# Optimization experiments

Measured on AMD Instinct MI355X. Metric: run time of the kernel, lower is better.

Reference implementation:

```python
import jax, jax.numpy as jnp
import numpy as np
import math

B, T, HIDDEN = 1, 2048, 2048
N_HEADS, N_KV = 16, 8
HD = HIDDEN // N_HEADS  # 128
EPS = 1e-6
THETA = 1e6


def _rmsnorm(x, w, eps=EPS):
    return x * jax.lax.rsqrt(jnp.mean(x * x, axis=-1, keepdims=True) + eps) * w


def _rope(x, sin, cos):
    # even/odd split, non-interleaved concat output (matches get_rope)
    x1 = x[..., 0::2]
    x2 = x[..., 1::2]
    s = sin[None, :, None, :]  # [1, T, 1, HD//2]
    c = cos[None, :, None, :]
    return jnp.concatenate([x1 * c - x2 * s, x1 * s + x2 * c], axis=-1)


def setup_inputs() -> dict:
    key = jax.random.key(0)
    ks = jax.random.split(key, 6)
    x = jax.random.normal(ks[0], (B, T, HIDDEN), dtype=jnp.float32)
    Wq = 0.02 * jax.random.normal(ks[1], (HIDDEN, 2 * HIDDEN), dtype=jnp.float32)
    Wk = 0.02 * jax.random.normal(ks[2], (HIDDEN, N_KV * HD), dtype=jnp.float32)
    Wv = 0.02 * jax.random.normal(ks[3], (HIDDEN, N_KV * HD), dtype=jnp.float32)
    Wo = 0.02 * jax.random.normal(ks[4], (2 * HIDDEN, HIDDEN), dtype=jnp.float32)
    q_norm_w = jnp.ones((2 * HD,), dtype=jnp.float32)
    k_norm_w = jnp.ones((HD,), dtype=jnp.float32)
    inv_freq = 1.0 / (THETA ** (jnp.arange(0, HD, 2, dtype=jnp.float32) / HD))
    freqs = jnp.arange(T, dtype=jnp.float32)[:, None] * inv_freq[None, :]  # [T, HD//2]
    return {"x": x, "Wq": Wq, "Wk": Wk, "Wv": Wv, "Wo": Wo,
            "q_norm_w": q_norm_w, "k_norm_w": k_norm_w,
            "sin": jnp.sin(freqs), "cos": jnp.cos(freqs)}


def reference(x, Wq, Wk, Wv, Wo, q_norm_w, k_norm_w, sin, cos):
    b, t, _ = x.shape
    # projections
    q = (x @ Wq).reshape(b, t, N_HEADS, 2 * HD)
    k = (x @ Wk).reshape(b, t, N_KV, HD)
    v = (x @ Wv).reshape(b, t, N_KV, HD)
    # per-head QK RMSNorm (q_norm over 2*head_dim)
    q = _rmsnorm(q, q_norm_w)
    k = _rmsnorm(k, k_norm_w)
    # split q into 2*N_HEADS attention heads of dim HD, apply RoPE
    hq = 2 * N_HEADS
    q = _rope(q.reshape(b, t, hq, HD), sin, cos)
    k = _rope(k, sin, cos)
    # GQA: repeat kv heads
    g = hq // N_KV
    k = jnp.repeat(k, g, axis=2)  # [b, t, hq, HD]
    v = jnp.repeat(v, g, axis=2)
    # attention: no causal mask in the original module
    att = jnp.einsum('bqhd,bkhd->bhqk', q, k) / math.sqrt(HD)
    p = jax.nn.softmax(att, axis=-1)
    out = jnp.einsum('bhqk,bkhd->bqhd', p, v).reshape(b, t, hq * HD)
    return out @ Wo
```

## Files before the change

kernel.cpp:

```cpp
#include <hip/hip_runtime.h>

typedef unsigned short u16;
typedef __attribute__((ext_vector_type(8))) short bf16x8;
typedef __attribute__((ext_vector_type(4))) short s16x4;
typedef __attribute__((ext_vector_type(4))) float f32x4;

__device__ __forceinline__ float bf2f(u16 u) {
  union { unsigned u; float f; } c; c.u = ((unsigned)u) << 16; return c.f;
}
__device__ __forceinline__ u16 f2bf(float f) {
  union { float f; unsigned u; } c; c.f = f;
  return (u16)((c.u + 0x7fffu + ((c.u >> 16) & 1u)) >> 16);
}
#if __has_builtin(__builtin_amdgcn_cvt_pk_bf16_f32)
__device__ __forceinline__ unsigned pkbf(float a, float b) {
  auto v = __builtin_amdgcn_cvt_pk_bf16_f32(a, b);
  return __builtin_bit_cast(unsigned, v);
}
#else
__device__ __forceinline__ unsigned pkbf(float a, float b) {
  return (unsigned)f2bf(a) | ((unsigned)f2bf(b) << 16);
}
#endif
#if __has_builtin(__builtin_amdgcn_mfma_f32_16x16x16bf16_1k)
#define MFMA16(a, b, c) __builtin_amdgcn_mfma_f32_16x16x16bf16_1k(a, b, c, 0, 0, 0)
#define HAVE_MFMA16 1
#endif
#if __has_builtin(__builtin_amdgcn_exp2f)
#define EXP2(x) __builtin_amdgcn_exp2f(x)
#else
#define EXP2(x) __expf((x) * 0.69314718f)
#endif
__device__ __forceinline__ void gl2lds16(const u16* g, u16* l) {
  __builtin_amdgcn_global_load_lds(
      (const __attribute__((address_space(1))) void*)g,
      (__attribute__((address_space(3))) void*)l, 16, 0, 0);
}

__device__ __forceinline__ void tr_cast_tile(const float* __restrict__ in,
                                             u16* __restrict__ out,
                                             int ldin, int ldout, int bx, int by) {
  __shared__ u16 tile[64][66];
  const int tx = threadIdx.x;
  const int lr = tx & 31, lc = tx >> 5;
  const int r0 = by << 6, c0 = bx << 6;
#pragma unroll
  for (int i = 0; i < 8; ++i) {
    int r = lc + (i << 3);
    float2 v = *(const float2*)&in[(size_t)(r0 + r) * ldin + c0 + (lr << 1)];
    *(unsigned*)&tile[r][lr << 1] = pkbf(v.x, v.y);
  }
  __syncthreads();
#pragma unroll
  for (int i = 0; i < 8; ++i) {
    int c = lc + (i << 3);
    unsigned v = (unsigned)tile[lr << 1][c] | ((unsigned)tile[(lr << 1) + 1][c] << 16);
    *(unsigned*)&out[(size_t)(c0 + c) * ldout + r0 + (lr << 1)] = v;
  }
}

__global__ __launch_bounds__(256) void prep(const float* __restrict__ x,
                                            u16* __restrict__ xb,
                                            const float* __restrict__ Wq,
                                            u16* __restrict__ WqT,
                                            const float* __restrict__ Wk,
                                            u16* __restrict__ WkT,
                                            const float* __restrict__ Wv,
                                            u16* __restrict__ WvT) {
  int b = blockIdx.x;
  if (b < 2048) {
    int i = (b * 256 + threadIdx.x) * 8;
    float4 a = *(const float4*)&x[i];
    float4 c = *(const float4*)&x[i + 4];
    union { unsigned u[4]; bf16x8 v; } w;
    w.u[0] = pkbf(a.x, a.y); w.u[1] = pkbf(a.z, a.w);
    w.u[2] = pkbf(c.x, c.y); w.u[3] = pkbf(c.z, c.w);
    *(bf16x8*)&xb[i] = w.v;
  } else if (b < 4096) {
    int t = b - 2048;
    tr_cast_tile(Wq, WqT, 4096, 2048, t & 63, t >> 6);
  } else if (b < 4608) {
    int t = b - 4096;
    tr_cast_tile(Wk, WkT, 1024, 2048, t & 15, t >> 4);
  } else {
    int t = b - 4608;
    tr_cast_tile(Wv, WvT, 1024, 2048, t & 15, t >> 4);
  }
}

__global__ __launch_bounds__(256) void transpose_cast(const float* __restrict__ in,
                                                      u16* __restrict__ out,
                                                      int ldin, int ldout) {
  tr_cast_tile(in, out, ldin, ldout, blockIdx.x, blockIdx.y);
}

__global__ __launch_bounds__(256) void gemm_bt(const u16* __restrict__ A,
                                               const u16* __restrict__ BT,
                                               u16* __restrict__ C,
                                               int M, int N, int K) {
  __shared__ u16 Asl[2][128 * 32];
  __shared__ u16 Bsl[2][128 * 32];
  const int tid = threadIdx.x;
  const int lane = tid & 63, wv = tid >> 6;
  const int lr = lane & 15, qd = lane >> 4;
  const int wr = wv >> 1, wc = wv & 1;
  const int m0 = blockIdx.y << 7, n0 = blockIdx.x << 7;
  const int srow = lane >> 2, scol = (lane & 3) << 3;
  const u16* Ag = &A[(size_t)(m0 + wv * 32 + srow) * K + scol];
  const u16* Bg = &BT[(size_t)(n0 + wv * 32 + srow) * K + scol];
  const size_t rstr16 = (size_t)16 * K;
  f32x4 acc[4][4] = {};
  for (int k0 = 0; k0 < K; k0 += 64) {
    __syncthreads();
#pragma unroll
    for (int p = 0; p < 2; ++p) {
#pragma unroll
      for (int hh = 0; hh < 2; ++hh) {
        gl2lds16(Ag + k0 + p * 32 + hh * rstr16, &Asl[p][wv * 1024 + hh * 512]);
        gl2lds16(Bg + k0 + p * 32 + hh * rstr16, &Bsl[p][wv * 1024 + hh * 512]);
      }
    }
    __syncthreads();
#pragma unroll
    for (int p = 0; p < 2; ++p) {
      bf16x8 af[4], bfr[4];
#pragma unroll
      for (int i = 0; i < 4; ++i) {
        af[i]  = *(const bf16x8*)&Asl[p][(wr * 64 + i * 16 + lr) * 32 + qd * 8];
        bfr[i] = *(const bf16x8*)&Bsl[p][(wc * 64 + i * 16 + lr) * 32 + qd * 8];
      }
#pragma unroll
      for (int mi = 0; mi < 4; ++mi)
#pragma unroll
        for (int ni = 0; ni < 4; ++ni)
          acc[mi][ni] = __builtin_amdgcn_mfma_f32_16x16x32_bf16(
              af[mi], bfr[ni], acc[mi][ni], 0, 0, 0);
    }
  }
#pragma unroll
  for (int mi = 0; mi < 4; ++mi)
#pragma unroll
    for (int ni = 0; ni < 4; ++ni)
#pragma unroll
      for (int r = 0; r < 4; ++r)
        C[(size_t)(m0 + wr * 64 + mi * 16 + qd * 4 + r) * N +
          n0 + wc * 64 + ni * 16 + lr] = f2bf(acc[mi][ni][r]);
}

__global__ __launch_bounds__(256) void gemm_bt_sk(const u16* __restrict__ A,
                                                  const u16* __restrict__ BT,
                                                  float* __restrict__ C,
                                                  int M, int N, int K, int kspan) {
  __shared__ u16 Asl[2][128 * 32];
  __shared__ u16 Bsl[2][128 * 32];
  const int tid = threadIdx.x;
  const int lane = tid & 63, wv = tid >> 6;
  const int lr = lane & 15, qd = lane >> 4;
  const int wr = wv >> 1, wc = wv & 1;
  const int m0 = blockIdx.y << 7, n0 = blockIdx.x << 7;
  const int kbeg = blockIdx.z * kspan;
  const int srow = lane >> 2, scol = (lane & 3) << 3;
  const u16* Ag = &A[(size_t)(m0 + wv * 32 + srow) * K + kbeg + scol];
  const u16* Bg = &BT[(size_t)(n0 + wv * 32 + srow) * K + kbeg + scol];
  const size_t rstr16 = (size_t)16 * K;
  f32x4 acc[4][4] = {};
  for (int k0 = 0; k0 < kspan; k0 += 64) {
    __syncthreads();
#pragma unroll
    for (int p = 0; p < 2; ++p) {
#pragma unroll
      for (int hh = 0; hh < 2; ++hh) {
        gl2lds16(Ag + k0 + p * 32 + hh * rstr16, &Asl[p][wv * 1024 + hh * 512]);
        gl2lds16(Bg + k0 + p * 32 + hh * rstr16, &Bsl[p][wv * 1024 + hh * 512]);
      }
    }
    __syncthreads();
#pragma unroll
    for (int p = 0; p < 2; ++p) {
      bf16x8 af[4], bfr[4];
#pragma unroll
      for (int i = 0; i < 4; ++i) {
        af[i]  = *(const bf16x8*)&Asl[p][(wr * 64 + i * 16 + lr) * 32 + qd * 8];
        bfr[i] = *(const bf16x8*)&Bsl[p][(wc * 64 + i * 16 + lr) * 32 + qd * 8];
      }
#pragma unroll
      for (int mi = 0; mi < 4; ++mi)
#pragma unroll
        for (int ni = 0; ni < 4; ++ni)
          acc[mi][ni] = __builtin_amdgcn_mfma_f32_16x16x32_bf16(
              af[mi], bfr[ni], acc[mi][ni], 0, 0, 0);
    }
  }
#pragma unroll
  for (int mi = 0; mi < 4; ++mi)
#pragma unroll
    for (int ni = 0; ni < 4; ++ni)
#pragma unroll
      for (int r = 0; r < 4; ++r)
        unsafeAtomicAdd(&C[(size_t)(m0 + wr * 64 + mi * 16 + qd * 4 + r) * N +
                           n0 + wc * 64 + ni * 16 + lr], acc[mi][ni][r]);
}

__global__ __launch_bounds__(256) void norm_vt(u16* __restrict__ QKV,
                                               u16* __restrict__ VTb,
                                               const float* __restrict__ qw,
                                               const float* __restrict__ kw,
                                               const float* __restrict__ sinb,
                                               const float* __restrict__ cosb) {
  int b = blockIdx.x;
  if (b >= 2048) {
    __shared__ u16 tile[64][66];
    int t = b - 2048;
    const int tx = threadIdx.x;
    const int lr = tx & 31, lc = tx >> 5;
    const int r0 = (t >> 4) << 6, c0 = (t & 15) << 6;
    const u16* in = QKV + 5120;
#pragma unroll
    for (int i = 0; i < 8; ++i) {
      int r = lc + (i << 3);
      unsigned v = *(const unsigned*)&in[(size_t)(r0 + r) * 6144 + c0 + (lr << 1)];
      *(unsigned*)&tile[r][lr << 1] = v;
    }
    __syncthreads();
#pragma unroll
    for (int i = 0; i < 8; ++i) {
      int c = lc + (i << 3);
      unsigned v = (unsigned)tile[lr << 1][c] | ((unsigned)tile[(lr << 1) + 1][c] << 16);
      *(unsigned*)&VTb[(size_t)(c0 + c) * 2048 + r0 + (lr << 1)] = v;
    }
    return;
  }
  const int t = b;
  const int wv = threadIdx.x >> 6, l = threadIdx.x & 63;
  const float sv = sinb[t * 64 + l];
  const float cv = cosb[t * 64 + l];
  const float qscale = 0.12753102543f;
  u16* Q = QKV + (size_t)t * 6144;
  u16* Kb = Q + 4096;
  for (int j = wv; j < 16; j += 4) {
    u16* base = Q + j * 256;
    float x0 = bf2f(base[2 * l]);
    float x1 = bf2f(base[2 * l + 1]);
    float x2 = bf2f(base[128 + 2 * l]);
    float x3 = bf2f(base[129 + 2 * l]);
    float ss = x0 * x0 + x1 * x1 + x2 * x2 + x3 * x3;
#pragma unroll
    for (int m = 1; m < 64; m <<= 1) ss += __shfl_xor(ss, m, 64);
    float rn = rsqrtf(ss * (1.0f / 256.0f) + 1e-6f);
    float w0 = qw[2 * l], w1 = qw[2 * l + 1];
    float w2 = qw[128 + 2 * l], w3 = qw[129 + 2 * l];
    x0 *= rn * w0; x1 *= rn * w1; x2 *= rn * w2; x3 *= rn * w3;
    base[l]       = f2bf((x0 * cv - x1 * sv) * qscale);
    base[64 + l]  = f2bf((x0 * sv + x1 * cv) * qscale);
    base[128 + l] = f2bf((x2 * cv - x3 * sv) * qscale);
    base[192 + l] = f2bf((x2 * sv + x3 * cv) * qscale);
  }
  for (int j = wv; j < 8; j += 4) {
    u16* base = Kb + j * 128;
    float x0 = bf2f(base[2 * l]);
    float x1 = bf2f(base[2 * l + 1]);
    float ss = x0 * x0 + x1 * x1;
#pragma unroll
    for (int m = 1; m < 64; m <<= 1) ss += __shfl_xor(ss, m, 64);
    float rn = rsqrtf(ss * (1.0f / 128.0f) + 1e-6f);
    float w0 = kw[2 * l], w1 = kw[2 * l + 1];
    x0 *= rn * w0; x1 *= rn * w1;
    base[l]      = f2bf(x0 * cv - x1 * sv);
    base[64 + l] = f2bf(x0 * sv + x1 * cv);
  }
}

__global__ __launch_bounds__(256, 2) void flash(const u16* __restrict__ QKV,
                                                const u16* __restrict__ VTb,
                                                u16* __restrict__ O0,
                                                u16* __restrict__ O1,
                                                float* __restrict__ L0,
                                                float* __restrict__ L1) {
  __shared__ u16 Ksl[64 * 128];
  __shared__ u16 Vsl[128 * 64];
  const int tid = threadIdx.x;
  const int wv = tid >> 6, lane = tid & 63;
  const int c = lane & 15, qd = lane >> 4;
  const int h = blockIdx.y, kv = h >> 2;
  const int qb = (blockIdx.x << 7) + wv * 32;
  const int z = blockIdx.z;
  u16* Ob = z ? O1 : O0;
  float* Lb = z ? L1 : L0;
  const int cx = c & 7;
  const int krow_off = lane >> 4;
  const int kpb = lane & 15;
  const int vrow_off = lane >> 3;
  const int vpb = lane & 7;
  bf16x8 qf[2][4];
#pragma unroll
  for (int ms = 0; ms < 2; ++ms)
#pragma unroll
    for (int ks = 0; ks < 4; ++ks)
      qf[ms][ks] = *(const bf16x8*)&QKV[(size_t)(qb + ms * 16 + c) * 6144 +
                                        h * 128 + ks * 32 + qd * 8];
  f32x4 o[2][8] = {};
  float lrun[2] = {0.f, 0.f};

  const int kbeg = z << 10, kend = kbeg + 1024;
  for (int k0 = kbeg; k0 < kend; k0 += 64) {
    __syncthreads();
#pragma unroll
    for (int it = 0; it < 4; ++it) {
      int rbase = (wv * 4 + it) * 4;
      int r = rbase + krow_off;
      int klb = kpb ^ (r & 7);
      gl2lds16(&QKV[(size_t)(k0 + r) * 6144 + 4096 + kv * 128 + klb * 8],
               &Ksl[rbase * 128]);
      int dbase = (wv * 4 + it) * 8;
      int d = dbase + vrow_off;
      int vlb = vpb ^ (d & 7);
      gl2lds16(&VTb[(size_t)(kv * 128 + d) * 2048 + k0 + vlb * 8],
               &Vsl[dbase * 64]);
    }
    __syncthreads();
    f32x4 s[2][4];
#pragma unroll
    for (int ns = 0; ns < 4; ++ns) {
      f32x4 a0 = {0.f, 0.f, 0.f, 0.f}, a1 = {0.f, 0.f, 0.f, 0.f};
#pragma unroll
      for (int ks = 0; ks < 4; ++ks) {
        bf16x8 kf = *(const bf16x8*)
            &Ksl[(ns * 16 + c) * 128 + (((4 * ks + qd) ^ cx) << 3)];
        a0 = __builtin_amdgcn_mfma_f32_16x16x32_bf16(kf, qf[0][ks], a0, 0, 0, 0);
        a1 = __builtin_amdgcn_mfma_f32_16x16x32_bf16(kf, qf[1][ks], a1, 0, 0, 0);
      }
      s[0][ns] = a0; s[1][ns] = a1;
    }
#pragma unroll
    for (int ms = 0; ms < 2; ++ms) {
      float rs = 0.f;
#pragma unroll
      for (int ns = 0; ns < 4; ++ns)
#pragma unroll
        for (int r = 0; r < 4; ++r) {
          float p = EXP2(s[ms][ns][r]);
          s[ms][ns][r] = p; rs += p;
        }
      lrun[ms] += rs;
    }
#ifdef HAVE_MFMA16
#pragma unroll
    for (int ns = 0; ns < 4; ++ns) {
      s16x4 pb[2];
#pragma unroll
      for (int ms = 0; ms < 2; ++ms) {
        union { unsigned u[2]; s16x4 v; } pu;
        pu.u[0] = pkbf(s[ms][ns][0], s[ms][ns][1]);
        pu.u[1] = pkbf(s[ms][ns][2], s[ms][ns][3]);
        pb[ms] = pu.v;
      }
      const int voff = ((((2 * ns) + (qd >> 1)) ^ cx) << 3) + (qd & 1) * 4;
#pragma unroll
      for (int n8 = 0; n8 < 8; ++n8) {
        s16x4 vf = *(const s16x4*)&Vsl[(n8 * 16 + c) * 64 + voff];
        o[0][n8] = MFMA16(vf, pb[0], o[0][n8]);
        o[1][n8] = MFMA16(vf, pb[1], o[1][n8]);
      }
    }
#else
    unsigned pk[2][4][2];
#pragma unroll
    for (int ms = 0; ms < 2; ++ms)
#pragma unroll
      for (int ns = 0; ns < 4; ++ns) {
        pk[ms][ns][0] = pkbf(s[ms][ns][0], s[ms][ns][1]);
        pk[ms][ns][1] = pkbf(s[ms][ns][2], s[ms][ns][3]);
      }
    const bool hi = lane >= 32;
    const int sl0 = ((lane >> 4) & 1) * 32 + c;
    const int sl1 = sl0 + 16;
#pragma unroll
    for (int t2 = 0; t2 < 2; ++t2) {
      union { int i[4]; bf16x8 v; } pb[2];
#pragma unroll
      for (int ms = 0; ms < 2; ++ms)
#pragma unroll
        for (int dw = 0; dw < 4; ++dw) {
          int rg = dw & 1;
          int sl = dw < 2 ? sl0 : sl1;
          int va = __shfl((int)pk[ms][2 * t2][rg], sl, 64);
          int vb = __shfl((int)pk[ms][2 * t2 + 1][rg], sl, 64);
          pb[ms].i[dw] = hi ? vb : va;
        }
#pragma unroll
      for (int n8 = 0; n8 < 8; ++n8) {
        bf16x8 vf = *(const bf16x8*)
            &Vsl[(n8 * 16 + c) * 64 + (((4 * t2 + qd) ^ cx) << 3)];
        o[0][n8] = __builtin_amdgcn_mfma_f32_16x16x32_bf16(vf, pb[0].v, o[0][n8], 0, 0, 0);
        o[1][n8] = __builtin_amdgcn_mfma_f32_16x16x32_bf16(vf, pb[1].v, o[1][n8], 0, 0, 0);
      }
    }
#endif
  }
#pragma unroll
  for (int ms = 0; ms < 2; ++ms) {
    lrun[ms] += __shfl_xor(lrun[ms], 16, 64);
    lrun[ms] += __shfl_xor(lrun[ms], 32, 64);
  }
  if (qd == 0) {
    Lb[(qb + c) * 32 + h] = lrun[0];
    Lb[(qb + 16 + c) * 32 + h] = lrun[1];
  }
#pragma unroll
  for (int ms = 0; ms < 2; ++ms)
#pragma unroll
    for (int n8 = 0; n8 < 8; ++n8) {
      union { unsigned u[2]; s16x4 v; } w;
      w.u[0] = pkbf(o[ms][n8][0], o[ms][n8][1]);
      w.u[1] = pkbf(o[ms][n8][2], o[ms][n8][3]);
      *(s16x4*)&Ob[(size_t)(qb + ms * 16 + c) * 4096 + h * 128 + n8 * 16 + qd * 4] = w.v;
    }
}

__global__ __launch_bounds__(256) void combine(u16* __restrict__ O0,
                                               const u16* __restrict__ O1,
                                               const float* __restrict__ L0,
                                               const float* __restrict__ L1) {
  int i8 = (blockIdx.x * 256 + threadIdx.x) * 8;
  int q = i8 >> 12, h = (i8 >> 7) & 31;
  float inv = 1.0f / (L0[q * 32 + h] + L1[q * 32 + h]);
  bf16x8 a = *(bf16x8*)&O0[i8];
  bf16x8 b = *(const bf16x8*)&O1[i8];
  union { unsigned u[4]; bf16x8 v; } w;
#pragma unroll
  for (int j = 0; j < 4; ++j) {
    float e0 = (bf2f((u16)a[2 * j]) + bf2f((u16)b[2 * j])) * inv;
    float e1 = (bf2f((u16)a[2 * j + 1]) + bf2f((u16)b[2 * j + 1])) * inv;
    w.u[j] = pkbf(e0, e1);
  }
  *(bf16x8*)&O0[i8] = w.v;
}

extern "C" void kernel_launch(void* const* d_in, const int* in_sizes, int n_in,
                              void* d_out, int out_size, void* d_ws, size_t ws_size,
                              hipStream_t stream) {
  const float* x    = (const float*)d_in[0];
  const float* Wq   = (const float*)d_in[1];
  const float* Wk   = (const float*)d_in[2];
  const float* Wv   = (const float*)d_in[3];
  const float* Wo   = (const float*)d_in[4];
  const float* qnw  = (const float*)d_in[5];
  const float* knw  = (const float*)d_in[6];
  const float* sinb = (const float*)d_in[7];
  const float* cosb = (const float*)d_in[8];
  float* out = (float*)d_out;
  char* ws = (char*)d_ws;
  const size_t MB = 1024 * 1024;
  u16* WqkvT = (u16*)(ws + 0 * MB);
  u16* Op0   = (u16*)(ws + 0 * MB);
  float* L0f = (float*)(ws + 16 * MB);
  float* L1f = (float*)(ws + 16 * MB + 262144);
  u16* QKV = (u16*)(ws + 24 * MB);
  u16* WoT = (u16*)(ws + 24 * MB);
  u16* xb  = (u16*)(ws + 48 * MB);
  u16* Op1 = (u16*)(ws + 48 * MB);
  u16* VTb = (u16*)(ws + 64 * MB);

  prep<<<5120, 256, 0, stream>>>(x, xb, Wq, WqkvT,
                                 Wk, WqkvT + (size_t)4096 * 2048,
                                 Wv, WqkvT + (size_t)5120 * 2048);
  gemm_bt<<<dim3(48, 16), 256, 0, stream>>>(xb, WqkvT, QKV, 2048, 6144, 2048);
  norm_vt<<<2560, 256, 0, stream>>>(QKV, VTb, qnw, knw, sinb, cosb);
  flash<<<dim3(16, 32, 2), 256, 0, stream>>>(QKV, VTb, Op0, Op1, L0f, L1f);
  transpose_cast<<<dim3(32, 64), 256, 0, stream>>>(Wo, WoT, 2048, 4096);
  combine<<<4096, 256, 0, stream>>>(Op0, Op1, L0f, L1f);
  hipMemsetAsync(out, 0, (size_t)2048 * 2048 * 4, stream);
  gemm_bt_sk<<<dim3(16, 16, 2), 256, 0, stream>>>(Op0, WoT, out, 2048, 2048, 4096, 2048);
  (void)in_sizes; (void)n_in; (void)out_size; (void)ws_size;
}
```

Measured before the change: 380.4 us.

## Double-buffer K/V tiles in flash kernel and use permlane swaps for P operand

Splits the K/V LDS staging into two buffers so the next 64-key tile is loaded asynchronously while the current one is computed, removing the load-then-wait stall per iteration. Adds a permlane16/32 swap path that rearranges the softmax probabilities into the 16x16x32 MFMA B-operand layout, replacing the 16x16x16 MFMA path. Also raises wave priority around MFMA blocks. LDS use doubles to 64KB per block, which may reduce occupancy at two blocks per CU.

```diff
diff --git a/kernel.cpp b/kernel.cpp
--- a/kernel.cpp
+++ b/kernel.cpp
@@ -25,6 +25,18 @@
 #if __has_builtin(__builtin_amdgcn_mfma_f32_16x16x16bf16_1k)
 #define MFMA16(a, b, c) __builtin_amdgcn_mfma_f32_16x16x16bf16_1k(a, b, c, 0, 0, 0)
 #define HAVE_MFMA16 1
+#endif
+#if __has_builtin(__builtin_amdgcn_permlane16_swap) && \
+    __has_builtin(__builtin_amdgcn_permlane32_swap)
+#define HAVE_PLSWAP 1
+__device__ __forceinline__ void plswap32(unsigned& a, unsigned& b) {
+  auto r = __builtin_amdgcn_permlane32_swap(a, b, false, false);
+  a = r[0]; b = r[1];
+}
+__device__ __forceinline__ void plswap16(unsigned& a, unsigned& b) {
+  auto r = __builtin_amdgcn_permlane16_swap(a, b, false, false);
+  a = r[0]; b = r[1];
+}
 #endif
 #if __has_builtin(__builtin_amdgcn_exp2f)
 #define EXP2(x) __builtin_amdgcn_exp2f(x)
@@ -276,8 +288,10 @@
                                                 u16* __restrict__ O1,
                                                 float* __restrict__ L0,
                                                 float* __restrict__ L1) {
-  __shared__ u16 Ksl[64 * 128];
-  __shared__ u16 Vsl[128 * 64];
+  __shared__ u16 Ks0[64 * 128];
+  __shared__ u16 Ks1[64 * 128];
+  __shared__ u16 Vs0[128 * 64];
+  __shared__ u16 Vs1[128 * 64];
   const int tid = threadIdx.x;
   const int wv = tid >> 6, lane = tid & 63;
   const int c = lane & 15, qd = lane >> 4;
@@ -301,36 +315,38 @@
   f32x4 o[2][8] = {};
   float lrun[2] = {0.f, 0.f};
 
-  const int kbeg = z << 10, kend = kbeg + 1024;
-  for (int k0 = kbeg; k0 < kend; k0 += 64) {
-    __syncthreads();
+  auto stage = [&](int k0, u16* Kd, u16* Vd) {
 #pragma unroll
     for (int it = 0; it < 4; ++it) {
       int rbase = (wv * 4 + it) * 4;
       int r = rbase + krow_off;
       int klb = kpb ^ (r & 7);
       gl2lds16(&QKV[(size_t)(k0 + r) * 6144 + 4096 + kv * 128 + klb * 8],
-               &Ksl[rbase * 128]);
+               &Kd[rbase * 128]);
       int dbase = (wv * 4 + it) * 8;
       int d = dbase + vrow_off;
       int vlb = vpb ^ (d & 7);
       gl2lds16(&VTb[(size_t)(kv * 128 + d) * 2048 + k0 + vlb * 8],
-               &Vsl[dbase * 64]);
-    }
-    __syncthreads();
+               &Vd[dbase * 64]);
+    }
+  };
+
+  auto compute = [&](const u16* Ks, const u16* Vs) {
     f32x4 s[2][4];
+    __builtin_amdgcn_s_setprio(1);
 #pragma unroll
     for (int ns = 0; ns < 4; ++ns) {
       f32x4 a0 = {0.f, 0.f, 0.f, 0.f}, a1 = {0.f, 0.f, 0.f, 0.f};
 #pragma unroll
       for (int ks = 0; ks < 4; ++ks) {
         bf16x8 kf = *(const bf16x8*)
-            &Ksl[(ns * 16 + c) * 128 + (((4 * ks + qd) ^ cx) << 3)];
+            &Ks[(ns * 16 + c) * 128 + (((4 * ks + qd) ^ cx) << 3)];
         a0 = __builtin_amdgcn_mfma_f32_16x16x32_bf16(kf, qf[0][ks], a0, 0, 0, 0);
         a1 = __builtin_amdgcn_mfma_f32_16x16x32_bf16(kf, qf[1][ks], a1, 0, 0, 0);
       }
       s[0][ns] = a0; s[1][ns] = a1;
     }
+    __builtin_amdgcn_s_setprio(0);
 #pragma unroll
     for (int ms = 0; ms < 2; ++ms) {
       float rs = 0.f;
@@ -343,7 +359,33 @@
         }
       lrun[ms] += rs;
     }
-#ifdef HAVE_MFMA16
+#ifdef HAVE_PLSWAP
+#pragma unroll
+    for (int t2 = 0; t2 < 2; ++t2) {
+      bf16x8 pB[2];
+#pragma unroll
+      for (int ms = 0; ms < 2; ++ms) {
+        unsigned p0 = pkbf(s[ms][2 * t2][0],     s[ms][2 * t2][1]);
+        unsigned p1 = pkbf(s[ms][2 * t2][2],     s[ms][2 * t2][3]);
+        unsigned p2 = pkbf(s[ms][2 * t2 + 1][0], s[ms][2 * t2 + 1][1]);
+        unsigned p3 = pkbf(s[ms][2 * t2 + 1][2], s[ms][2 * t2 + 1][3]);
+        plswap32(p0, p2); plswap16(p0, p2);
+        plswap32(p1, p3); plswap16(p1, p3);
+        union { unsigned u[4]; bf16x8 v; } bb;
+        bb.u[0] = p0; bb.u[1] = p1; bb.u[2] = p2; bb.u[3] = p3;
+        pB[ms] = bb.v;
+      }
+      __builtin_amdgcn_s_setprio(1);
+#pragma unroll
+      for (int n8 = 0; n8 < 8; ++n8) {
+        bf16x8 vf = *(const bf16x8*)
+            &Vs[(n8 * 16 + c) * 64 + (((4 * t2 + qd) ^ cx) << 3)];
+        o[0][n8] = __builtin_amdgcn_mfma_f32_16x16x32_bf16(vf, pB[0], o[0][n8], 0, 0, 0);
+        o[1][n8] = __builtin_amdgcn_mfma_f32_16x16x32_bf16(vf, pB[1], o[1][n8], 0, 0, 0);
+      }
+      __builtin_amdgcn_s_setprio(0);
+    }
+#elif defined(HAVE_MFMA16)
 #pragma unroll
     for (int ns = 0; ns < 4; ++ns) {
       s16x4 pb[2];
@@ -357,7 +399,7 @@
       const int voff = ((((2 * ns) + (qd >> 1)) ^ cx) << 3) + (qd & 1) * 4;
 #pragma unroll
       for (int n8 = 0; n8 < 8; ++n8) {
-        s16x4 vf = *(const s16x4*)&Vsl[(n8 * 16 + c) * 64 + voff];
+        s16x4 vf = *(const s16x4*)&Vs[(n8 * 16 + c) * 64 + voff];
         o[0][n8] = MFMA16(vf, pb[0], o[0][n8]);
         o[1][n8] = MFMA16(vf, pb[1], o[1][n8]);
       }
@@ -390,12 +432,24 @@
 #pragma unroll
       for (int n8 = 0; n8 < 8; ++n8) {
         bf16x8 vf = *(const bf16x8*)
-            &Vsl[(n8 * 16 + c) * 64 + (((4 * t2 + qd) ^ cx) << 3)];
+            &Vs[(n8 * 16 + c) * 64 + (((4 * t2 + qd) ^ cx) << 3)];
         o[0][n8] = __builtin_amdgcn_mfma_f32_16x16x32_bf16(vf, pb[0].v, o[0][n8], 0, 0, 0);
         o[1][n8] = __builtin_amdgcn_mfma_f32_16x16x32_bf16(vf, pb[1].v, o[1][n8], 0, 0, 0);
       }
     }
 #endif
+  };
+
+  const int kbeg = z << 10, kend = kbeg + 1024;
+  stage(kbeg, Ks0, Vs0);
+#pragma unroll 1
+  for (int k0 = kbeg; k0 < kend; k0 += 128) {
+    __syncthreads();
+    stage(k0 + 64, Ks1, Vs1);
+    compute(Ks0, Vs0);
+    __syncthreads();
+    if (k0 + 128 < kend) stage(k0 + 128, Ks0, Vs0);
+    compute(Ks1, Vs1);
   }
 #pragma unroll
   for (int ms = 0; ms < 2; ++ms) {
```

After: 383.4 us. No clear change (+0.8%).
